# Kernel tuning notes

Hardware: AMD Instinct MI355X
Metric: run time of the kernel (lower is better)

Reference implementation:

```python
import math
import jax, jax.numpy as jnp
import numpy as np

B, L, IN_DIM, D, OUT_DIM = 4, 4096, 512, 64, 512


def setup_inputs() -> dict:
    key = jax.random.key(0)
    ks = jax.random.split(key, 9)
    s_in = 1.0 / math.sqrt(IN_DIM)
    s_d = 1.0 / math.sqrt(D)
    return {
        "x": jax.random.normal(ks[0], (B, L, IN_DIM), jnp.float32),
        "Wq": jax.random.normal(ks[1], (IN_DIM, D), jnp.float32) * s_in,
        "bq": jax.random.normal(ks[2], (D,), jnp.float32) * s_in,
        "Wk": jax.random.normal(ks[3], (IN_DIM, D), jnp.float32) * s_in,
        "bk": jax.random.normal(ks[4], (D,), jnp.float32) * s_in,
        "Wv": jax.random.normal(ks[5], (IN_DIM, D), jnp.float32) * s_in,
        "bv": jax.random.normal(ks[6], (D,), jnp.float32) * s_in,
        "Wo": jax.random.normal(ks[7], (D, OUT_DIM), jnp.float32) * s_d,
        "bo": jax.random.normal(ks[8], (OUT_DIM,), jnp.float32) * s_d,
    }


def reference(x, Wq, bq, Wk, bk, Wv, bv, Wo, bo):
    # q, k, v: [B, L, D]
    q = x @ Wq + bq
    k = x @ Wk + bk
    v = x @ Wv + bv
    scale = 1.0 / math.sqrt(D)
    # scores: [B, Lq, Lk]
    scores = jnp.einsum("bqd,bkd->bqk", q, k) * scale
    # NOTE: original uses nn.Softmax(dim=1) -> softmax over the QUERY axis (axis=1)
    attention = jax.nn.softmax(scores, axis=1)
    values_with_attention = jnp.einsum("bqk,bkd->bqd", attention, v)
    output = values_with_attention @ Wo + bo
    return (output, attention)
```

## Files before the change

kernel.cpp:

```cpp
#include <hip/hip_runtime.h>
#include <hip/hip_fp16.h>
#include <math.h>

#define Bdim 4
#define Lseq 4096
#define INDIM 512
#define DH 64
#define OUTD 512
#define SCALE 0.125f
#define KSPL 8
#define QSPL 8
#define BL (Bdim * Lseq)

typedef _Float16 f16;
typedef _Float16 h8 __attribute__((ext_vector_type(8)));
typedef _Float16 h4 __attribute__((ext_vector_type(4)));
typedef float f4 __attribute__((ext_vector_type(4)));

#define MFMA(a, b, c) __builtin_amdgcn_mfma_f32_16x16x32_f16(a, b, c, 0, 0, 0)

__global__ __launch_bounds__(256) void wtrans(const float* __restrict__ Wq,
                                              const float* __restrict__ Wk,
                                              const float* __restrict__ Wv,
                                              f16* __restrict__ whi,
                                              f16* __restrict__ wlo) {
    __shared__ float tile[64 * 68];
    int t = threadIdx.x;
    int kt = blockIdx.x * 64;
    const float* W = (blockIdx.y == 0) ? Wq : (blockIdx.y == 1) ? Wk : Wv;
    {
        int r = t >> 2, c4 = (t & 3) * 16;
        const float4* src = (const float4*)(W + (size_t)(kt + r) * DH + c4);
#pragma unroll
        for (int i = 0; i < 4; ++i)
            *(float4*)(tile + r * 68 + c4 + 4 * i) = src[i];
    }
    __syncthreads();
    {
        int d = t >> 2, k8 = (t & 3) * 16;
        h8 hi0, hi1, lo0, lo1;
#pragma unroll
        for (int j = 0; j < 8; ++j) {
            float v0 = tile[(k8 + j) * 68 + d];
            float v1 = tile[(k8 + 8 + j) * 68 + d];
            f16 h0 = (f16)v0, h1 = (f16)v1;
            hi0[j] = h0; lo0[j] = (f16)(v0 - (float)h0);
            hi1[j] = h1; lo1[j] = (f16)(v1 - (float)h1);
        }
        size_t base = ((size_t)blockIdx.y * DH + d) * INDIM + kt + k8;
        *(h8*)(whi + base) = hi0;
        *(h8*)(whi + base + 8) = hi1;
        *(h8*)(wlo + base) = lo0;
        *(h8*)(wlo + base + 8) = lo1;
    }
}

__global__ __launch_bounds__(256) void proj_qkv(const float* __restrict__ x,
                                                const f16* __restrict__ whi,
                                                const f16* __restrict__ wlo,
                                                const float* __restrict__ bq,
                                                const float* __restrict__ bk,
                                                const float* __restrict__ bv,
                                                f16* __restrict__ qh,
                                                f16* __restrict__ kh,
                                                f16* __restrict__ vt) {
    __shared__ __align__(16) f16 xh[64 * 72];
    __shared__ __align__(16) f16 xl[64 * 72];
    __shared__ __align__(16) f16 wl[6][64 * 72];
    int t = threadIdx.x;
    int w = t >> 6, lane = t & 63;
    int l15 = lane & 15, quad = lane >> 4;
    size_t row0 = (size_t)blockIdx.x * 64;

    int xr = t >> 2, xkq = (t & 3) * 16;
    int wd = t >> 2, wko = (t & 3) * 16;

    f4 acc[3][4];
#pragma unroll
    for (int m = 0; m < 3; ++m)
#pragma unroll
        for (int nt = 0; nt < 4; ++nt) acc[m][nt] = (f4){0.f, 0.f, 0.f, 0.f};

    f4 xs[4];
    h8 wsr[12];

#define PROJ_ISSUE(kc)                                                             \
    {                                                                              \
        const f4* xsrc = (const f4*)(x + (row0 + xr) * INDIM + (kc) + xkq);        \
        _Pragma("unroll") for (int i = 0; i < 4; ++i) xs[i] = xsrc[i];             \
        _Pragma("unroll") for (int p = 0; p < 6; ++p) {                            \
            const f16* src = ((p & 1) ? wlo : whi) +                               \
                             ((size_t)(p >> 1) * DH + wd) * INDIM + (kc) + wko;    \
            wsr[p * 2] = *(const h8*)src;                                          \
            wsr[p * 2 + 1] = *(const h8*)(src + 8);                                \
        }                                                                          \
    }

#define PROJ_COMMIT()                                                              \
    {                                                                              \
        h8 hi0, hi1, lo0, lo1;                                                     \
        _Pragma("unroll") for (int j = 0; j < 4; ++j) {                            \
            _Pragma("unroll") for (int i = 0; i < 2; ++i) {                        \
                float v0 = xs[i][j + 0] , v1 = xs[i][j]; (void)v1;                 \
            }                                                                      \
        }                                                                          \
        _Pragma("unroll") for (int j = 0; j < 8; ++j) {                            \
            float v0 = ((const float*)xs)[j];                                      \
            float v1 = ((const float*)xs)[8 + j];                                  \
            f16 h0 = (f16)v0, h1 = (f16)v1;                                        \
            hi0[j] = h0; lo0[j] = (f16)(v0 - (float)h0);                           \
            hi1[j] = h1; lo1[j] = (f16)(v1 - (float)h1);                           \
        }                                                                          \
        *(h8*)(xh + xr * 72 + xkq) = hi0;                                          \
        *(h8*)(xh + xr * 72 + xkq + 8) = hi1;                                      \
        *(h8*)(xl + xr * 72 + xkq) = lo0;                                          \
        *(h8*)(xl + xr * 72 + xkq + 8) = lo1;                                      \
        _Pragma("unroll") for (int p = 0; p < 6; ++p) {                            \
            *(h8*)(wl[p] + wd * 72 + wko) = wsr[p * 2];                            \
            *(h8*)(wl[p] + wd * 72 + wko + 8) = wsr[p * 2 + 1];                    \
        }                                                                          \
    }

    PROJ_ISSUE(0);
    PROJ_COMMIT();
    __syncthreads();

    int arow = w * 16 + l15;
    for (int it = 0; it < 8; ++it) {
        if (it < 7) PROJ_ISSUE((it + 1) * 64);

        h8 ah0 = *(const h8*)(xh + arow * 72 + quad * 8);
        h8 ah1 = *(const h8*)(xh + arow * 72 + 32 + quad * 8);
        h8 al0 = *(const h8*)(xl + arow * 72 + quad * 8);
        h8 al1 = *(const h8*)(xl + arow * 72 + 32 + quad * 8);
#pragma unroll
        for (int m = 0; m < 3; ++m) {
            const f16* bh = wl[m * 2];
            const f16* bl = wl[m * 2 + 1];
#pragma unroll
            for (int nt = 0; nt < 4; ++nt) {
                int d = nt * 16 + l15;
                h8 bh0 = *(const h8*)(bh + d * 72 + quad * 8);
                h8 bh1 = *(const h8*)(bh + d * 72 + 32 + quad * 8);
                h8 bl0 = *(const h8*)(bl + d * 72 + quad * 8);
                h8 bl1 = *(const h8*)(bl + d * 72 + 32 + quad * 8);
                f4 c = acc[m][nt];
                c = MFMA(ah0, bh0, c);
                c = MFMA(ah1, bh1, c);
                c = MFMA(al0, bh0, c);
                c = MFMA(al1, bh1, c);
                c = MFMA(ah0, bl0, c);
                c = MFMA(ah1, bl1, c);
                acc[m][nt] = c;
            }
        }
        __syncthreads();
        if (it < 7) PROJ_COMMIT();
        __syncthreads();
    }

    int b = (int)(row0 >> 12);
    int kr0 = ((int)row0 & (Lseq - 1)) + w * 16 + quad * 4;
#pragma unroll
    for (int nt = 0; nt < 4; ++nt) {
        int d = nt * 16 + l15;
        float bqv = bq[d], bkv = bk[d], bvv = bv[d];
#pragma unroll
        for (int reg = 0; reg < 4; ++reg) {
            size_t r = row0 + w * 16 + quad * 4 + reg;
            qh[r * DH + d] = (f16)((acc[0][nt][reg] + bqv) * SCALE);
            kh[r * DH + d] = (f16)(acc[1][nt][reg] + bkv);
        }
        h4 pv;
#pragma unroll
        for (int reg = 0; reg < 4; ++reg) pv[reg] = (f16)(acc[2][nt][reg] + bvv);
        *(h4*)(vt + ((size_t)b * DH + d) * Lseq + kr0) = pv;
    }
#undef PROJ_ISSUE
#undef PROJ_COMMIT
}

__global__ __launch_bounds__(256) void col_stats(const f16* __restrict__ qh,
                                                 const f16* __restrict__ kh,
                                                 float* __restrict__ lsum) {
    __shared__ __align__(16) f16 qlds[2][64 * 72];
    int t = threadIdx.x;
    int w = t >> 6, lane = t & 63;
    int l15 = lane & 15, quad = lane >> 4;
    int b = blockIdx.y;
    int kblk = blockIdx.x * 128;
    int qbase = blockIdx.z * (Lseq / QSPL);

    h8 a[2][2];
#pragma unroll
    for (int kt = 0; kt < 2; ++kt) {
        const h8* kr = (const h8*)(kh + ((size_t)b * Lseq + kblk + w * 32 + kt * 16 + l15) * DH + quad * 8);
        a[kt][0] = kr[0];
        a[kt][1] = kr[4];
    }
    float lp[2][4] = {};

#pragma unroll
    for (int i = 0; i < 2; ++i) {
        int lin = i * 256 + t;
        int row = lin >> 3, c8 = lin & 7;
        *(h8*)(qlds[0] + row * 72 + c8 * 8) =
            *(const h8*)(qh + ((size_t)b * Lseq + qbase + row) * DH + c8 * 8);
    }
    __syncthreads();

    for (int it = 0; it < (Lseq / QSPL) / 64; ++it) {
        h8 s0, s1;
        int r0_ = 0, c0_ = 0, r1_ = 0, c1_ = 0;
        if (it < 7) {
            int lin0 = t, lin1 = 256 + t;
            r0_ = lin0 >> 3; c0_ = lin0 & 7;
            r1_ = lin1 >> 3; c1_ = lin1 & 7;
            s0 = *(const h8*)(qh + ((size_t)b * Lseq + qbase + (it + 1) * 64 + r0_) * DH + c0_ * 8);
            s1 = *(const h8*)(qh + ((size_t)b * Lseq + qbase + (it + 1) * 64 + r1_) * DH + c1_ * 8);
        }
        const f16* qb = qlds[it & 1];
#pragma unroll
        for (int nt = 0; nt < 4; ++nt) {
            const f16* qp = qb + (nt * 16 + l15) * 72 + quad * 8;
            h8 b0 = *(const h8*)qp;
            h8 b1 = *(const h8*)(qp + 32);
#pragma unroll
            for (int kt = 0; kt < 2; ++kt) {
                f4 c = {0.f, 0.f, 0.f, 0.f};
                c = MFMA(a[kt][0], b0, c);
                c = MFMA(a[kt][1], b1, c);
#pragma unroll
                for (int reg = 0; reg < 4; ++reg) lp[kt][reg] += __expf(c[reg]);
            }
        }
        if (it < 7) {
            f16* qn = qlds[(it & 1) ^ 1];
            *(h8*)(qn + r0_ * 72 + c0_ * 8) = s0;
            *(h8*)(qn + r1_ * 72 + c1_ * 8) = s1;
        }
        __syncthreads();
    }
#pragma unroll
    for (int kt = 0; kt < 2; ++kt)
#pragma unroll
        for (int reg = 0; reg < 4; ++reg) {
            float v = lp[kt][reg];
            v += __shfl_xor(v, 1);
            v += __shfl_xor(v, 2);
            v += __shfl_xor(v, 4);
            v += __shfl_xor(v, 8);
            if (l15 == 0)
                atomicAdd(&lsum[(size_t)b * Lseq + kblk + w * 32 + kt * 16 + quad * 4 + reg], v);
        }
}

__global__ __launch_bounds__(256, 4) void attn_pv(const f16* __restrict__ qh,
                                                  const f16* __restrict__ kh,
                                                  const f16* __restrict__ vt,
                                                  const float* __restrict__ lsum,
                                                  float* __restrict__ att,
                                                  f16* __restrict__ opart) {
    __shared__ __align__(16) f16 klds[2][64 * 72];
    __shared__ __align__(16) f16 es[4][32 * 80];
    int t = threadIdx.x;
    int w = t >> 6, lane = t & 63;
    int l15 = lane & 15, quad = lane >> 4;
    int b = blockIdx.y;
    int q0 = blockIdx.x * 128 + w * 32;
    int split = blockIdx.z;
    int kstart = split * (Lseq / KSPL);

    h8 aq[2][2];
#pragma unroll
    for (int mt = 0; mt < 2; ++mt) {
        const h8* qp = (const h8*)(qh + ((size_t)b * Lseq + q0 + mt * 16 + l15) * DH + quad * 8);
        aq[mt][0] = qp[0];
        aq[mt][1] = qp[4];
    }
    f4 o[2][4];
#pragma unroll
    for (int mt = 0; mt < 2; ++mt)
#pragma unroll
        for (int nt = 0; nt < 4; ++nt) o[mt][nt] = (f4){0.f, 0.f, 0.f, 0.f};

    const float* lsb = lsum + (size_t)b * Lseq;
    f16* ew = es[w];

#pragma unroll
    for (int i = 0; i < 2; ++i) {
        int lin = i * 256 + t;
        int row = lin >> 3, c8 = lin & 7;
        *(h8*)(klds[0] + row * 72 + c8 * 8) =
            *(const h8*)(kh + ((size_t)b * Lseq + kstart + row) * DH + c8 * 8);
    }
    __syncthreads();

    for (int it = 0; it < 8; ++it) {
        int kbase = kstart + it * 64;
        const f16* kb = klds[it & 1];

        h8 s0, s1;
        int r0_ = 0, c0_ = 0, r1_ = 0, c1_ = 0;
        if (it < 7) {
            int lin0 = t, lin1 = 256 + t;
            r0_ = lin0 >> 3; c0_ = lin0 & 7;
            r1_ = lin1 >> 3; c1_ = lin1 & 7;
            s0 = *(const h8*)(kh + ((size_t)b * Lseq + kbase + 64 + r0_) * DH + c0_ * 8);
            s1 = *(const h8*)(kh + ((size_t)b * Lseq + kbase + 64 + r1_) * DH + c1_ * 8);
        }

#pragma unroll
        for (int nt = 0; nt < 4; ++nt) {
            const f16* kp = kb + (nt * 16 + l15) * 72 + quad * 8;
            h8 b0 = *(const h8*)kp;
            h8 b1 = *(const h8*)(kp + 32);
            float rlv = 1.0f / lsb[kbase + nt * 16 + l15];
#pragma unroll
            for (int mt = 0; mt < 2; ++mt) {
                f4 c = {0.f, 0.f, 0.f, 0.f};
                c = MFMA(aq[mt][0], b0, c);
                c = MFMA(aq[mt][1], b1, c);
#pragma unroll
                for (int reg = 0; reg < 4; ++reg)
                    ew[(mt * 16 + quad * 4 + reg) * 80 + nt * 16 + l15] =
                        (f16)(__expf(c[reg]) * rlv);
            }
        }

        {
            int g = lane >> 3, c8 = lane & 7;
#pragma unroll
            for (int rr = 0; rr < 4; ++rr) {
                int row = rr * 8 + g;
                h8 hv = *(const h8*)(ew + row * 80 + c8 * 8);
                f4 v0, v1;
#pragma unroll
                for (int j = 0; j < 4; ++j) {
                    v0[j] = (float)hv[j];
                    v1[j] = (float)hv[4 + j];
                }
                float* dst = att + ((size_t)b * Lseq + q0 + row) * Lseq + kbase + c8 * 8;
                *(f4*)dst = v0;
                *(f4*)(dst + 4) = v1;
            }
        }

        h8 ae[2][2];
#pragma unroll
        for (int mt = 0; mt < 2; ++mt) {
            const f16* ep = ew + (mt * 16 + l15) * 80 + quad * 8;
            ae[mt][0] = *(const h8*)ep;
            ae[mt][1] = *(const h8*)(ep + 32);
        }
#pragma unroll
        for (int nt = 0; nt < 4; ++nt) {
            const h8* vp = (const h8*)(vt + ((size_t)b * DH + nt * 16 + l15) * Lseq + kbase + quad * 8);
            h8 bv0 = vp[0];
            h8 bv1 = vp[4];
            o[0][nt] = MFMA(ae[0][0], bv0, o[0][nt]);
            o[0][nt] = MFMA(ae[0][1], bv1, o[0][nt]);
            o[1][nt] = MFMA(ae[1][0], bv0, o[1][nt]);
            o[1][nt] = MFMA(ae[1][1], bv1, o[1][nt]);
        }

        if (it < 7) {
            f16* kn = klds[(it & 1) ^ 1];
            *(h8*)(kn + r0_ * 72 + c0_ * 8) = s0;
            *(h8*)(kn + r1_ * 72 + c1_ * 8) = s1;
        }
        __syncthreads();
    }

#pragma unroll
    for (int mt = 0; mt < 2; ++mt)
#pragma unroll
        for (int nt = 0; nt < 4; ++nt)
#pragma unroll
            for (int reg = 0; reg < 4; ++reg) {
                size_t qrow = (size_t)b * Lseq + q0 + mt * 16 + quad * 4 + reg;
                opart[((size_t)split * BL + qrow) * DH + nt * 16 + l15] = (f16)o[mt][nt][reg];
            }
}

#define WOFF(c) ((c) * 8 + ((c) >> 2) * 4)

__global__ __launch_bounds__(256) void out_proj(const f16* __restrict__ opart,
                                                const float* __restrict__ Wo,
                                                const float* __restrict__ bo,
                                                float* __restrict__ out) {
    __shared__ float osT[64 * 68];
    __shared__ float wos[64 * 144];
    int t = threadIdx.x;
    int rg = blockIdx.x, oq = blockIdx.y;
#pragma unroll
    for (int j = 0; j < 8; ++j) {
        int idx = j * 256 + t;
        int dd = idx >> 5, c4b = idx & 31;
        int c8b = c4b >> 1, half = (c4b & 1) * 4;
        *(float4*)(wos + dd * 144 + WOFF(c8b) + half) =
            *(const float4*)(Wo + (size_t)dd * OUTD + oq * 128 + c4b * 4);
    }
    {
        int row = t >> 2, dq = (t & 3) * 16;
        float s[16] = {};
#pragma unroll
        for (int sp = 0; sp < KSPL; ++sp) {
            const h8* src = (const h8*)(opart + ((size_t)sp * BL + (size_t)rg * 64 + row) * DH + dq);
            h8 v0 = src[0], v1 = src[1];
#pragma unroll
            for (int jj = 0; jj < 8; ++jj) {
                s[jj] += (float)v0[jj];
                s[8 + jj] += (float)v1[jj];
            }
        }
#pragma unroll
        for (int jj = 0; jj < 16; ++jj) osT[(dq + jj) * 68 + row] = s[jj];
    }
    __syncthreads();
    int r4 = t >> 4, c8 = t & 15;
    float acc[4][8] = {};
#pragma unroll 8
    for (int dd = 0; dd < DH; ++dd) {
        f4 ov = *(f4*)(osT + dd * 68 + r4 * 4);
        f4 w0 = *(f4*)(wos + dd * 144 + WOFF(c8));
        f4 w1 = *(f4*)(wos + dd * 144 + WOFF(c8) + 4);
#pragma unroll
        for (int i = 0; i < 4; ++i)
#pragma unroll
            for (int j = 0; j < 4; ++j) {
                acc[i][j]     += ov[i] * w0[j];
                acc[i][4 + j] += ov[i] * w1[j];
            }
    }
    f4 b0 = *(const f4*)(bo + oq * 128 + c8 * 8);
    f4 b1 = *(const f4*)(bo + oq * 128 + c8 * 8 + 4);
#pragma unroll
    for (int i = 0; i < 4; ++i) {
        size_t row = (size_t)rg * 64 + r4 * 4 + i;
        f4 r0, r1;
#pragma unroll
        for (int j = 0; j < 4; ++j) {
            r0[j] = acc[i][j] + b0[j];
            r1[j] = acc[i][4 + j] + b1[j];
        }
        *(f4*)(out + row * OUTD + oq * 128 + c8 * 8) = r0;
        *(f4*)(out + row * OUTD + oq * 128 + c8 * 8 + 4) = r1;
    }
}

extern "C" void kernel_launch(void* const* d_in, const int* in_sizes, int n_in,
                              void* d_out, int out_size, void* d_ws, size_t ws_size,
                              hipStream_t stream) {
    const float* x  = (const float*)d_in[0];
    const float* Wq = (const float*)d_in[1];
    const float* bq = (const float*)d_in[2];
    const float* Wk = (const float*)d_in[3];
    const float* bk = (const float*)d_in[4];
    const float* Wv = (const float*)d_in[5];
    const float* bv = (const float*)d_in[6];
    const float* Wo = (const float*)d_in[7];
    const float* bo = (const float*)d_in[8];

    float* out = (float*)d_out;
    float* att = out + (size_t)BL * OUTD;

    char* ws = (char*)d_ws;
    f16*   qh    = (f16*)(ws + 0);
    f16*   kh    = (f16*)(ws + (size_t)(2 << 20));
    f16*   vt    = (f16*)(ws + (size_t)(4 << 20));
    float* lsum  = (float*)(ws + (size_t)(6 << 20));
    f16*   opart = (f16*)(ws + (size_t)(7 << 20));
    f16*   whi   = (f16*)(ws + (size_t)(23 << 20));
    f16*   wlo   = (f16*)(ws + (size_t)(23 << 20) + (size_t)(192 << 10));

    hipMemsetAsync(lsum, 0, (size_t)BL * sizeof(float), stream);
    wtrans<<<dim3(INDIM / 64, 3), 256, 0, stream>>>(Wq, Wk, Wv, whi, wlo);
    proj_qkv<<<dim3(BL / 64), 256, 0, stream>>>(x, whi, wlo, bq, bk, bv, qh, kh, vt);
    col_stats<<<dim3(Lseq / 128, Bdim, QSPL), 256, 0, stream>>>(qh, kh, lsum);
    attn_pv<<<dim3(Lseq / 128, Bdim, KSPL), 256, 0, stream>>>(qh, kh, vt, lsum, att, opart);
    out_proj<<<dim3(BL / 64, OUTD / 128), 256, 0, stream>>>(opart, Wo, bo, out);
}
```

Baseline: 424.2 us.

## Move output projection to split-fp16 MFMA and raise wave priority around MFMA loops

The output projection now runs on 16x16x32 f16 MFMA using a hi/lo split of both the reduced attention output and a pre-transposed Wo, replacing the scalar fp32 FMA loop. Wo is converted and transposed once in the extended wtrans kernel. s_setprio hints are also added around MFMA sections in col_stats, attn_pv and out_proj, and a dead loop in the projection commit is removed. The split-fp16 scheme keeps roughly fp32 accuracy at three MFMAs per product, and the output stores become scalar 4-byte writes instead of float4 writes.

After: 423.3 us (median of 2 runs). Within noise of the previous version (-0.2%).

```diff
diff --git a/kernel.cpp b/kernel.cpp
--- a/kernel.cpp
+++ b/kernel.cpp
@@ -22,36 +22,68 @@
 __global__ __launch_bounds__(256) void wtrans(const float* __restrict__ Wq,
                                               const float* __restrict__ Wk,
                                               const float* __restrict__ Wv,
+                                              const float* __restrict__ Wo,
                                               f16* __restrict__ whi,
-                                              f16* __restrict__ wlo) {
+                                              f16* __restrict__ wlo,
+                                              f16* __restrict__ woth,
+                                              f16* __restrict__ wotl) {
     __shared__ float tile[64 * 68];
     int t = threadIdx.x;
-    int kt = blockIdx.x * 64;
-    const float* W = (blockIdx.y == 0) ? Wq : (blockIdx.y == 1) ? Wk : Wv;
-    {
-        int r = t >> 2, c4 = (t & 3) * 16;
-        const float4* src = (const float4*)(W + (size_t)(kt + r) * DH + c4);
-#pragma unroll
-        for (int i = 0; i < 4; ++i)
-            *(float4*)(tile + r * 68 + c4 + 4 * i) = src[i];
-    }
-    __syncthreads();
-    {
-        int d = t >> 2, k8 = (t & 3) * 16;
-        h8 hi0, hi1, lo0, lo1;
-#pragma unroll
-        for (int j = 0; j < 8; ++j) {
-            float v0 = tile[(k8 + j) * 68 + d];
-            float v1 = tile[(k8 + 8 + j) * 68 + d];
-            f16 h0 = (f16)v0, h1 = (f16)v1;
-            hi0[j] = h0; lo0[j] = (f16)(v0 - (float)h0);
-            hi1[j] = h1; lo1[j] = (f16)(v1 - (float)h1);
-        }
-        size_t base = ((size_t)blockIdx.y * DH + d) * INDIM + kt + k8;
-        *(h8*)(whi + base) = hi0;
-        *(h8*)(whi + base + 8) = hi1;
-        *(h8*)(wlo + base) = lo0;
-        *(h8*)(wlo + base + 8) = lo1;
+    if (blockIdx.y < 3) {
+        int kt = blockIdx.x * 64;
+        const float* W = (blockIdx.y == 0) ? Wq : (blockIdx.y == 1) ? Wk : Wv;
+        {
+            int r = t >> 2, c4 = (t & 3) * 16;
+            const float4* src = (const float4*)(W + (size_t)(kt + r) * DH + c4);
+#pragma unroll
+            for (int i = 0; i < 4; ++i)
+                *(float4*)(tile + r * 68 + c4 + 4 * i) = src[i];
+        }
+        __syncthreads();
+        {
+            int d = t >> 2, k8 = (t & 3) * 16;
+            h8 hi0, hi1, lo0, lo1;
+#pragma unroll
+            for (int j = 0; j < 8; ++j) {
+                float v0 = tile[(k8 + j) * 68 + d];
+                float v1 = tile[(k8 + 8 + j) * 68 + d];
+                f16 h0 = (f16)v0, h1 = (f16)v1;
+                hi0[j] = h0; lo0[j] = (f16)(v0 - (float)h0);
+                hi1[j] = h1; lo1[j] = (f16)(v1 - (float)h1);
+            }
+            size_t base = ((size_t)blockIdx.y * DH + d) * INDIM + kt + k8;
+            *(h8*)(whi + base) = hi0;
+            *(h8*)(whi + base + 8) = hi1;
+            *(h8*)(wlo + base) = lo0;
+            *(h8*)(wlo + base + 8) = lo1;
+        }
+    } else {
+        int o0 = blockIdx.x * 64;
+        {
+            int d = t >> 2, o4 = (t & 3) * 16;
+            const float4* src = (const float4*)(Wo + (size_t)d * OUTD + o0 + o4);
+#pragma unroll
+            for (int i = 0; i < 4; ++i)
+                *(float4*)(tile + d * 68 + o4 + 4 * i) = src[i];
+        }
+        __syncthreads();
+        {
+            int o = t >> 2, d8 = (t & 3) * 16;
+            h8 hi0, hi1, lo0, lo1;
+#pragma unroll
+            for (int j = 0; j < 8; ++j) {
+                float v0 = tile[(d8 + j) * 68 + o];
+                float v1 = tile[(d8 + 8 + j) * 68 + o];
+                f16 h0 = (f16)v0, h1 = (f16)v1;
+                hi0[j] = h0; lo0[j] = (f16)(v0 - (float)h0);
+                hi1[j] = h1; lo1[j] = (f16)(v1 - (float)h1);
+            }
+            size_t base = (size_t)(o0 + o) * DH + d8;
+            *(h8*)(woth + base) = hi0;
+            *(h8*)(woth + base + 8) = hi1;
+            *(h8*)(wotl + base) = lo0;
+            *(h8*)(wotl + base + 8) = lo1;
+        }
     }
 }
 
@@ -99,11 +131,6 @@
 #define PROJ_COMMIT()                                                              \
     {                                                                              \
         h8 hi0, hi1, lo0, lo1;                                                     \
-        _Pragma("unroll") for (int j = 0; j < 4; ++j) {                            \
-            _Pragma("unroll") for (int i = 0; i < 2; ++i) {                        \
-                float v0 = xs[i][j + 0] , v1 = xs[i][j]; (void)v1;                 \
-            }                                                                      \
-        }                                                                          \
         _Pragma("unroll") for (int j = 0; j < 8; ++j) {                            \
             float v0 = ((const float*)xs)[j];                                      \
             float v1 = ((const float*)xs)[8 + j];                                  \
@@ -220,6 +247,7 @@
             s1 = *(const h8*)(qh + ((size_t)b * Lseq + qbase + (it + 1) * 64 + r1_) * DH + c1_ * 8);
         }
         const f16* qb = qlds[it & 1];
+        __builtin_amdgcn_s_setprio(1);
 #pragma unroll
         for (int nt = 0; nt < 4; ++nt) {
             const f16* qp = qb + (nt * 16 + l15) * 72 + quad * 8;
@@ -234,6 +262,7 @@
                 for (int reg = 0; reg < 4; ++reg) lp[kt][reg] += __expf(c[reg]);
             }
         }
+        __builtin_amdgcn_s_setprio(0);
         if (it < 7) {
             f16* qn = qlds[(it & 1) ^ 1];
             *(h8*)(qn + r0_ * 72 + c0_ * 8) = s0;
@@ -316,6 +345,7 @@
             h8 b0 = *(const h8*)kp;
             h8 b1 = *(const h8*)(kp + 32);
             float rlv = 1.0f / lsb[kbase + nt * 16 + l15];
+            __builtin_amdgcn_s_setprio(1);
 #pragma unroll
             for (int mt = 0; mt < 2; ++mt) {
                 f4 c = {0.f, 0.f, 0.f, 0.f};
@@ -326,6 +356,7 @@
                     ew[(mt * 16 + quad * 4 + reg) * 80 + nt * 16 + l15] =
                         (f16)(__expf(c[reg]) * rlv);
             }
+            __builtin_amdgcn_s_setprio(0);
         }
 
         {
@@ -353,6 +384,7 @@
             ae[mt][0] = *(const h8*)ep;
             ae[mt][1] = *(const h8*)(ep + 32);
         }
+        __builtin_amdgcn_s_setprio(1);
 #pragma unroll
         for (int nt = 0; nt < 4; ++nt) {
             const h8* vp = (const h8*)(vt + ((size_t)b * DH + nt * 16 + l15) * Lseq + kbase + quad * 8);
@@ -363,6 +395,7 @@
             o[1][nt] = MFMA(ae[1][0], bv0, o[1][nt]);
             o[1][nt] = MFMA(ae[1][1], bv1, o[1][nt]);
         }
+        __builtin_amdgcn_s_setprio(0);
 
         if (it < 7) {
             f16* kn = klds[(it & 1) ^ 1];
@@ -383,24 +416,19 @@
             }
 }
 
-#define WOFF(c) ((c) * 8 + ((c) >> 2) * 4)
-
 __global__ __launch_bounds__(256) void out_proj(const f16* __restrict__ opart,
-                                                const float* __restrict__ Wo,
+                                                const f16* __restrict__ woth,
+                                                const f16* __restrict__ wotl,
                                                 const float* __restrict__ bo,
                                                 float* __restrict__ out) {
-    __shared__ float osT[64 * 68];
-    __shared__ float wos[64 * 144];
+    __shared__ __align__(16) f16 osh[64 * 72];
+    __shared__ __align__(16) f16 osl[64 * 72];
     int t = threadIdx.x;
-    int rg = blockIdx.x, oq = blockIdx.y;
-#pragma unroll
-    for (int j = 0; j < 8; ++j) {
-        int idx = j * 256 + t;
-        int dd = idx >> 5, c4b = idx & 31;
-        int c8b = c4b >> 1, half = (c4b & 1) * 4;
-        *(float4*)(wos + dd * 144 + WOFF(c8b) + half) =
-            *(const float4*)(Wo + (size_t)dd * OUTD + oq * 128 + c4b * 4);
-    }
+    int w = t >> 6, lane = t & 63;
+    int l15 = lane & 15, quad = lane >> 4;
+    int rg = blockIdx.x;
+    int oq = blockIdx.y;
+
     {
         int row = t >> 2, dq = (t & 3) * 16;
         float s[16] = {};
@@ -414,38 +442,58 @@
                 s[8 + jj] += (float)v1[jj];
             }
         }
-#pragma unroll
-        for (int jj = 0; jj < 16; ++jj) osT[(dq + jj) * 68 + row] = s[jj];
+        h8 hi0, hi1, lo0, lo1;
+#pragma unroll
+        for (int jj = 0; jj < 8; ++jj) {
+            f16 h0 = (f16)s[jj], h1 = (f16)s[8 + jj];
+            hi0[jj] = h0; lo0[jj] = (f16)(s[jj] - (float)h0);
+            hi1[jj] = h1; lo1[jj] = (f16)(s[8 + jj] - (float)h1);
+        }
+        *(h8*)(osh + row * 72 + dq) = hi0;
+        *(h8*)(osh + row * 72 + dq + 8) = hi1;
+        *(h8*)(osl + row * 72 + dq) = lo0;
+        *(h8*)(osl + row * 72 + dq + 8) = lo1;
     }
     __syncthreads();
-    int r4 = t >> 4, c8 = t & 15;
-    float acc[4][8] = {};
-#pragma unroll 8
-    for (int dd = 0; dd < DH; ++dd) {
-        f4 ov = *(f4*)(osT + dd * 68 + r4 * 4);
-        f4 w0 = *(f4*)(wos + dd * 144 + WOFF(c8));
-        f4 w1 = *(f4*)(wos + dd * 144 + WOFF(c8) + 4);
-#pragma unroll
-        for (int i = 0; i < 4; ++i)
-#pragma unroll
-            for (int j = 0; j < 4; ++j) {
-                acc[i][j]     += ov[i] * w0[j];
-                acc[i][4 + j] += ov[i] * w1[j];
-            }
-    }
-    f4 b0 = *(const f4*)(bo + oq * 128 + c8 * 8);
-    f4 b1 = *(const f4*)(bo + oq * 128 + c8 * 8 + 4);
-#pragma unroll
-    for (int i = 0; i < 4; ++i) {
-        size_t row = (size_t)rg * 64 + r4 * 4 + i;
-        f4 r0, r1;
-#pragma unroll
-        for (int j = 0; j < 4; ++j) {
-            r0[j] = acc[i][j] + b0[j];
-            r1[j] = acc[i][4 + j] + b1[j];
-        }
-        *(f4*)(out + row * OUTD + oq * 128 + c8 * 8) = r0;
-        *(f4*)(out + row * OUTD + oq * 128 + c8 * 8 + 4) = r1;
+
+    int arow = w * 16 + l15;
+    h8 ah0 = *(const h8*)(osh + arow * 72 + quad * 8);
+    h8 ah1 = *(const h8*)(osh + arow * 72 + 32 + quad * 8);
+    h8 al0 = *(const h8*)(osl + arow * 72 + quad * 8);
+    h8 al1 = *(const h8*)(osl + arow * 72 + 32 + quad * 8);
+
+    f4 acc[8];
+#pragma unroll
+    for (int nt = 0; nt < 8; ++nt) acc[nt] = (f4){0.f, 0.f, 0.f, 0.f};
+
+    __builtin_amdgcn_s_setprio(1);
+#pragma unroll
+    for (int nt = 0; nt < 8; ++nt) {
+        int col = oq * 128 + nt * 16 + l15;
+        const h8* bh = (const h8*)(woth + (size_t)col * DH + quad * 8);
+        const h8* bl = (const h8*)(wotl + (size_t)col * DH + quad * 8);
+        h8 bh0 = bh[0], bh1 = bh[4];
+        h8 bl0 = bl[0], bl1 = bl[4];
+        f4 c = acc[nt];
+        c = MFMA(ah0, bh0, c);
+        c = MFMA(ah1, bh1, c);
+        c = MFMA(al0, bh0, c);
+        c = MFMA(al1, bh1, c);
+        c = MFMA(ah0, bl0, c);
+        c = MFMA(ah1, bl1, c);
+        acc[nt] = c;
+    }
+    __builtin_amdgcn_s_setprio(0);
+
+#pragma unroll
+    for (int nt = 0; nt < 8; ++nt) {
+        int col = oq * 128 + nt * 16 + l15;
+        float bov = bo[col];
+#pragma unroll
+        for (int reg = 0; reg < 4; ++reg) {
+            size_t row = (size_t)rg * 64 + w * 16 + quad * 4 + reg;
+            out[row * OUTD + col] = acc[nt][reg] + bov;
+        }
     }
 }
 
@@ -473,11 +521,13 @@
     f16*   opart = (f16*)(ws + (size_t)(7 << 20));
     f16*   whi   = (f16*)(ws + (size_t)(23 << 20));
     f16*   wlo   = (f16*)(ws + (size_t)(23 << 20) + (size_t)(192 << 10));
+    f16*   woth  = (f16*)(ws + (size_t)(23 << 20) + (size_t)(384 << 10));
+    f16*   wotl  = (f16*)(ws + (size_t)(23 << 20) + (size_t)(448 << 10));
 
     hipMemsetAsync(lsum, 0, (size_t)BL * sizeof(float), stream);
-    wtrans<<<dim3(INDIM / 64, 3), 256, 0, stream>>>(Wq, Wk, Wv, whi, wlo);
+    wtrans<<<dim3(8, 4), 256, 0, stream>>>(Wq, Wk, Wv, Wo, whi, wlo, woth, wotl);
     proj_qkv<<<dim3(BL / 64), 256, 0, stream>>>(x, whi, wlo, bq, bk, bv, qh, kh, vt);
     col_stats<<<dim3(Lseq / 128, Bdim, QSPL), 256, 0, stream>>>(qh, kh, lsum);
     attn_pv<<<dim3(Lseq / 128, Bdim, KSPL), 256, 0, stream>>>(qh, kh, vt, lsum, att, opart);
-    out_proj<<<dim3(BL / 64, OUTD / 128), 256, 0, stream>>>(opart, Wo, bo, out);
+    out_proj<<<dim3(BL / 64, OUTD / 128), 256, 0, stream>>>(opart, woth, wotl, bo, out);
 }
```
